# Performance work log

Measured on AMD Instinct MI355X. Metric: run time of the kernel, lower is better.

## Reference

```python
import jax, jax.numpy as jnp
import numpy as np

B, C, H = 256, 5, 13
N_AGENTS = 8192
N_EDGES = 262144
ACT = 21


def setup_inputs() -> dict:
    key = jax.random.key(0)
    ks = jax.random.split(key, 20)
    inp = {
        "x": jax.random.normal(ks[0], (B, C, H, H), jnp.float32),
        "x_msg": jax.random.normal(ks[1], (N_AGENTS,), jnp.float32),
        "edge_index": jax.random.randint(ks[2], (N_EDGES, 2), 0, N_AGENTS, jnp.int64 if jax.config.jax_enable_x64 else jnp.int32),
        "action": jax.random.randint(ks[3], (B,), 0, ACT, jnp.int32),
        # params (orthogonal init approximated by scaled normal; math identical)
        "conv1_w": jax.random.normal(ks[4], (32, 5, 3, 3), jnp.float32) * 0.1,
        "conv1_b": jnp.zeros((32,), jnp.float32),
        "conv2_w": jax.random.normal(ks[5], (64, 32, 3, 3), jnp.float32) * 0.05,
        "conv2_b": jnp.zeros((64,), jnp.float32),
        "fc_w": jax.random.normal(ks[6], (512, 1024), jnp.float32) * 0.03,
        "fc_b": jnp.zeros((512,), jnp.float32),
        "fc_mu_w": jax.random.normal(ks[7], (ACT, 512), jnp.float32) * 0.01,
        "fc_mu_b": jnp.zeros((ACT,), jnp.float32),
        "msg_w": jax.random.normal(ks[8], (N_AGENTS, 512), jnp.float32) * 0.01,
        "msg_b": jnp.zeros((N_AGENTS,), jnp.float32),
        "gcn1_w": jax.random.normal(ks[9], (2, 16), jnp.float32) * 0.5,
        "gcn1_b": jnp.zeros((16,), jnp.float32),
        "gcn2_w": jax.random.normal(ks[10], (16, N_AGENTS), jnp.float32) * 0.1,
        "gcn2_b": jnp.zeros((N_AGENTS,), jnp.float32),
    }
    return inp


def _gcn_norm(edge_index, n):
    # add self-loops; edge_index is (E,2) [src, dst]
    loops = jnp.arange(n, dtype=edge_index.dtype)
    src = jnp.concatenate([edge_index[:, 0], loops])
    dst = jnp.concatenate([edge_index[:, 1], loops])
    deg = jax.ops.segment_sum(jnp.ones_like(src, jnp.float32), dst, num_segments=n)
    dinv = jnp.where(deg > 0, jax.lax.rsqrt(deg), 0.0)
    norm = dinv[src] * dinv[dst]  # [E+n]
    return src, dst, norm


def _gcn_conv(h, src, dst, norm, W, b, n):
    hw = h @ W  # [n, out]
    out = jax.ops.segment_sum(norm[:, None] * hw[src], dst, num_segments=n)
    return out + b


def reference(x, x_msg, edge_index, action, conv1_w, conv1_b, conv2_w, conv2_b,
              fc_w, fc_b, fc_mu_w, fc_mu_b, msg_w, msg_b,
              gcn1_w, gcn1_b, gcn2_w, gcn2_b):
    dn = ("NCHW", "OIHW", "NCHW")
    h = jax.lax.conv_general_dilated(x, conv1_w, (2, 2), "VALID", dimension_numbers=dn)
    h = jax.nn.relu(h + conv1_b[None, :, None, None])  # [B,32,6,6]
    h = jax.lax.conv_general_dilated(h, conv2_w, (1, 1), "VALID", dimension_numbers=dn)
    h = jax.nn.relu(h + conv2_b[None, :, None, None])  # [B,64,4,4]
    h = h.reshape(h.shape[0], -1)  # [B,1024], torch NCHW flatten order
    hidden = jax.nn.relu(h @ fc_w.T + fc_b)  # [B,512]

    logits = hidden @ fc_mu_w.T + fc_mu_b            # [B,21]
    actor_encoding = hidden @ msg_w.T + msg_b        # [B,N]

    # Categorical log_prob / entropy for the given action
    logp = jax.nn.log_softmax(logits, axis=-1)
    log_prob = jnp.take_along_axis(logp, action[:, None], axis=1)[:, 0]
    entropy = -jnp.sum(jnp.exp(logp) * logp, axis=-1)

    # GNN message branch (eval mode: dropout is identity)
    feats = jnp.stack([x_msg, actor_encoding[0]], axis=0).T  # [N,2]
    n = feats.shape[0]
    src, dst, norm = _gcn_norm(edge_index, n)
    g = jax.nn.relu(_gcn_conv(feats, src, dst, norm, gcn1_w, gcn1_b, n))  # [N,16]
    g = _gcn_conv(g, src, dst, norm, gcn2_w, gcn2_b, n)                    # [N,N]
    msg_out = jax.nn.log_softmax(g, axis=1).mean(axis=1)                   # [N]

    return (action, msg_out, log_prob, entropy)
```

## Files before the change

kernel.cpp:

```cpp
#include <hip/hip_runtime.h>
#include <hip/hip_bf16.h>

#define NB 256
#define NACT 21
#define NA 8192
#define NE 262144
#define CSR_CAP 128
#define LOG2E 1.44269504f

#if __has_builtin(__builtin_amdgcn_exp2f)
#define EXP2F(x) __builtin_amdgcn_exp2f(x)
#else
#define EXP2F(x) exp2f(x)
#endif

typedef __attribute__((ext_vector_type(8))) short short8;
typedef __attribute__((ext_vector_type(4))) float float4v;

__device__ inline float wsum64(float v) {
#pragma unroll
  for (int m = 32; m > 0; m >>= 1) v += __shfl_xor(v, m, 64);
  return v;
}

__device__ inline unsigned short f2bf(float f) {
  union { __hip_bfloat16 h; unsigned short u; } cv;
  cv.h = __float2bfloat16(f);
  return cv.u;
}

__global__ void k_init(const int* action, int* cnt, float* out) {
  int i = blockIdx.x * 256 + threadIdx.x;
  if (i < NA) cnt[i] = 0;
  if (i < NB) out[i] = (float)action[i];
}

__global__ __launch_bounds__(512, 4) void k_prep(
    const int* __restrict__ edges, const float* __restrict__ fcw,
    const float* __restrict__ g2w, const float* __restrict__ g2b,
    unsigned short* fcwbf, unsigned short* w2t, float* wpart, int* cnt, int* csr) {
  __shared__ float red[16][17];
  __shared__ float b2s[16];
  int t = threadIdx.x, blk = blockIdx.x;
  {
    int e = blk * 512 + t;
    int s = edges[2 * e], d = edges[2 * e + 1];
    int slot = atomicAdd(&cnt[d], 1);
    if (slot < CSR_CAP) csr[d * CSR_CAP + slot] = s;
  }
  {
    int base = (blk * 512 + t) * 2;
    float2 v = *(const float2*)&fcw[base];
    fcwbf[base + 0] = f2bf(v.x);
    fcwbf[base + 1] = f2bf(v.y);
  }
  {
    if (t < 256) {
      int jj = t >> 4, k = t & 15;
      int j = blk * 16 + jj;
      float w = g2w[k * 8192 + j];
      w2t[j * 16 + k] = f2bf(w);
      red[jj][k] = w;
    }
    if (t < 16) b2s[t] = g2b[blk * 16 + t];
    __syncthreads();
    if (t < 16) {
      float s = 0.0f;
#pragma unroll
      for (int q = 0; q < 16; q++) s += red[q][t];
      wpart[blk * 17 + t] = s;
    } else if (t == 16) {
      float s = 0.0f;
#pragma unroll
      for (int q = 0; q < 16; q++) s += b2s[q];
      wpart[blk * 17 + 16] = s;
    }
  }
}

__global__ __launch_bounds__(512, 2) void k_conv(
    const float* __restrict__ x, const float* __restrict__ c1w, const float* __restrict__ c1b,
    const float* __restrict__ c2w, const float* __restrict__ c2b, unsigned short* h1024bf) {
  __shared__ float xs[845];
  __shared__ float w1s[1440];
  __shared__ float c1s[1152];
  __shared__ float w2s[64 * 73];
  int t = threadIdx.x, blk = blockIdx.x;
  for (int i = t; i < 845; i += 512) xs[i] = x[blk * 845 + i];
  for (int i = t; i < 1440; i += 512) w1s[i] = c1w[i];
  __syncthreads();
  for (int idx = t; idx < 1152; idx += 512) {
    int oc = idx / 36, p = idx - oc * 36;
    int oy = p / 6, ox = p - oy * 6;
    float acc = c1b[oc];
    const float* wp = &w1s[oc * 45];
#pragma unroll
    for (int ic = 0; ic < 5; ic++)
#pragma unroll
      for (int ky = 0; ky < 3; ky++)
#pragma unroll
        for (int kx = 0; kx < 3; kx++)
          acc += xs[ic * 169 + (oy * 2 + ky) * 13 + ox * 2 + kx] * wp[ic * 9 + ky * 3 + kx];
    c1s[idx] = fmaxf(acc, 0.0f);
  }
  int p = t & 15, oc2 = t >> 4;
  int oy = p >> 2, ox = p & 3;
  float a0 = c2b[oc2 * 2 + 0], a1 = c2b[oc2 * 2 + 1];
  for (int icb = 0; icb < 32; icb += 8) {
    __syncthreads();
    for (int i = t; i < 4608; i += 512) {
      int oc = i / 72, r = i - oc * 72;
      w2s[oc * 73 + r] = c2w[oc * 288 + icb * 9 + r];
    }
    __syncthreads();
#pragma unroll
    for (int ic = 0; ic < 8; ic++) {
#pragma unroll
      for (int ky = 0; ky < 3; ky++) {
#pragma unroll
        for (int kx = 0; kx < 3; kx++) {
          float cvv = c1s[(icb + ic) * 36 + (oy + ky) * 6 + ox + kx];
          int wi = ic * 9 + ky * 3 + kx;
          a0 += cvv * w2s[(oc2 * 2 + 0) * 73 + wi];
          a1 += cvv * w2s[(oc2 * 2 + 1) * 73 + wi];
        }
      }
    }
  }
  unsigned short* hp = &h1024bf[blk * 1024];
  hp[(oc2 * 2 + 0) * 16 + p] = f2bf(fmaxf(a0, 0.0f));
  hp[(oc2 * 2 + 1) * 16 + p] = f2bf(fmaxf(a1, 0.0f));
}

__global__ __launch_bounds__(256, 4) void k_fc(
    const int* __restrict__ cnt, const float* __restrict__ x_msg,
    const unsigned short* __restrict__ h1024bf, const unsigned short* __restrict__ fcwbf,
    const float* __restrict__ fcb, float* hidden, float* dinv, float* xs2) {
  __shared__ float red[4][256];
  int t = threadIdx.x, blk = blockIdx.x;
  int wave = t >> 6, lane = t & 63;
  if (blk < 32) {
    int i = blk * 256 + t;
    float d = rsqrtf((float)cnt[i] + 1.0f);
    dinv[i] = d;
    xs2[i] = d * x_msg[i];
  }
  int tr = blk >> 5, tc = blk & 31;
  int m = lane & 15, quad = lane >> 4;
  const unsigned short* ap = &h1024bf[(tr * 16 + m) * 1024 + wave * 256 + quad * 8];
  const unsigned short* bp = &fcwbf[(tc * 16 + m) * 1024 + wave * 256 + quad * 8];
  float4v acc = {0.0f, 0.0f, 0.0f, 0.0f};
#pragma unroll
  for (int i = 0; i < 8; i++) {
    short8 a = *(const short8*)(ap + i * 32);
    short8 b = *(const short8*)(bp + i * 32);
    acc = __builtin_amdgcn_mfma_f32_16x16x32_bf16(a, b, acc, 0, 0, 0);
  }
#pragma unroll
  for (int r = 0; r < 4; r++) red[wave][(quad * 4 + r) * 16 + m] = acc[r];
  __syncthreads();
  {
    float s = red[0][t] + red[1][t] + red[2][t] + red[3][t];
    int gr = tr * 16 + (t >> 4);
    int gc = tc * 16 + (t & 15);
    hidden[gr * 512 + gc] = fmaxf(s + fcb[gc], 0.0f);
  }
}

__global__ __launch_bounds__(512, 2) void k_he(
    const float* __restrict__ hidden, const float* __restrict__ muw,
    const float* __restrict__ mub, const float* __restrict__ msgw,
    const float* __restrict__ msgb, const float* __restrict__ dinv,
    float* es2, float* out) {
  __shared__ float muT[10752];
  __shared__ float hrows[2048];
  int t = threadIdx.x, blk = blockIdx.x;
  int wave = t >> 6, lane = t & 63;
  if (blk < 64) {
    int b0 = blk * 4;
    for (int i = t; i < 10752; i += 512) {
      int a = i >> 9, k = i & 511;
      muT[k * 21 + a] = muw[i];
    }
    for (int i = t; i < 2048; i += 512) hrows[i] = hidden[b0 * 512 + i];
    __syncthreads();
    if (wave < 4) {
      int b = b0 + wave;
      float logit = -1e30f;
      if (lane < NACT) {
        float acc = mub[lane];
        const float* hr = &hrows[wave * 512];
        for (int k = 0; k < 512; k++) acc += hr[k] * muT[k * 21 + lane];
        logit = acc;
      }
      float m = logit;
#pragma unroll
      for (int s = 32; s > 0; s >>= 1) m = fmaxf(m, __shfl_xor(m, s, 64));
      float e = (lane < NACT) ? __expf(logit - m) : 0.0f;
      float se = wsum64(e);
      float swl = wsum64(e * logit);
      float lse = m + __logf(se);
      if (lane == 0) out[8704 + b] = lse - swl / se;
      int act = (int)out[b];
      if (lane == act) out[8448 + b] = logit - lse;
    }
  } else {
    int wg = (blk - 64) * 8 + wave;
    for (int j = wg; j < NA; j += 3584) {
      const float* wp = &msgw[j * 512 + lane * 8];
      float4 w0 = *(const float4*)(wp);
      float4 w1 = *(const float4*)(wp + 4);
      float4 h0 = *(const float4*)&hidden[lane * 8];
      float4 h1 = *(const float4*)&hidden[lane * 8 + 4];
      float s = w0.x * h0.x + w0.y * h0.y + w0.z * h0.z + w0.w * h0.w +
                w1.x * h1.x + w1.y * h1.y + w1.z * h1.z + w1.w * h1.w;
      s = wsum64(s);
      if (lane == 0) es2[j] = dinv[j] * (s + msgb[j]);
    }
  }
}

__global__ __launch_bounds__(512, 4) void k_g1(
    const int* __restrict__ cnt, const int* __restrict__ csr,
    const float* __restrict__ dinv, const float* __restrict__ xs2,
    const float* __restrict__ es2, const float* __restrict__ g1w,
    const float* __restrict__ g1b, float* gbuf2) {
  int t = threadIdx.x, blk = blockIdx.x;
  int wave = t >> 6, lane = t & 63;
  int wg = blk * 8 + wave;
#pragma unroll
  for (int rr = 0; rr < 2; rr++) {
    int i = wg * 2 + rr;
    int ci = min(cnt[i], CSR_CAP);
    float di = dinv[i];
    float a0 = 0.0f, a1 = 0.0f;
    for (int e = lane; e < ci; e += 64) {
      int s = csr[i * CSR_CAP + e];
      a0 += xs2[s];
      a1 += es2[s];
    }
    float f0 = (wsum64(a0) + xs2[i]) * di;
    float f1 = (wsum64(a1) + es2[i]) * di;
    if (lane < 16) {
      float gv = fmaxf(f0 * g1w[lane] + f1 * g1w[16 + lane] + g1b[lane], 0.0f);
      gbuf2[i * 16 + lane] = di * gv;
    }
  }
}

__global__ __launch_bounds__(512, 2) void k_msg(
    const int* __restrict__ cnt, const int* __restrict__ csr,
    const float* __restrict__ dinv, const float* __restrict__ gbuf2,
    const float* __restrict__ wpart, const unsigned short* __restrict__ w2t,
    const float* __restrict__ g2b, float* out) {
  __shared__ __align__(16) unsigned short vbf[512];
  __shared__ float vf[512];
  __shared__ float pl[4096];
  __shared__ float sl[256];
  __shared__ float wp[16][17];
  __shared__ float wsf[17];
  int t = threadIdx.x, blk = blockIdx.x;
  int wave = t >> 6, lane = t & 63;
  int rowbase = blk * 32;
  {
    int eq = lane >> 4, c = lane & 15;
#pragma unroll
    for (int rr = 0; rr < 4; rr++) {
      int il = wave * 4 + rr;
      int i = rowbase + il;
      int ci = min(cnt[i], CSR_CAP);
      float di = dinv[i];
      float acc = (eq == 0) ? gbuf2[i * 16 + c] : 0.0f;
      for (int e = eq; e < ci; e += 4) {
        int s = csr[i * CSR_CAP + e];
        acc += gbuf2[s * 16 + c];
      }
      acc *= di;
      acc += __shfl_xor(acc, 16, 64);
      acc += __shfl_xor(acc, 32, 64);
      if (eq == 0) {
        vf[il * 16 + c] = acc;
        vbf[il * 16 + c] = f2bf(acc * LOG2E);
      }
    }
  }
  __syncthreads();
  if (t < 272) {
    int bq = t / 17, k = t - bq * 17;
    float s = 0.0f;
    for (int b = bq; b < 512; b += 16) s += wpart[b * 17 + k];
    wp[bq][k] = s;
  }
  __syncthreads();
  if (t < 17) {
    float s = 0.0f;
#pragma unroll
    for (int q = 0; q < 16; q++) s += wp[q][t];
    wsf[t] = s;
  }
  __syncthreads();
  float myMean = 0.0f;
  if (t < 32) {
    float dot = 0.0f;
#pragma unroll
    for (int c = 0; c < 16; c++) dot += vf[t * 16 + c] * wsf[c];
    myMean = (dot + wsf[16]) * (1.0f / 8192.0f);
  }
  {
    int quad = lane >> 4, n = lane & 15;
    int k8 = quad * 8;
    short8 za = {0, 0, 0, 0, 0, 0, 0, 0};
    short8 a1 = za, a2 = za;
    if (quad < 2) {
      a1 = *(const short8*)&vbf[n * 16 + k8];
      a2 = *(const short8*)&vbf[(16 + n) * 16 + k8];
    }
    float sacc[8];
#pragma unroll
    for (int q = 0; q < 8; q++) sacc[q] = 0.0f;
    int colb = wave * 1024 + n;
    for (int tp = 0; tp < 64; tp += 2) {
      int col1 = colb + tp * 16;
      int col2 = col1 + 16;
      short8 b1 = za, b2 = za;
      if (quad < 2) {
        b1 = *(const short8*)&w2t[col1 * 16 + k8];
        b2 = *(const short8*)&w2t[col2 * 16 + k8];
      }
      float bb1 = g2b[col1] * LOG2E, bb2 = g2b[col2] * LOG2E;
      float4v c1 = {bb1, bb1, bb1, bb1};
      float4v c2 = {bb2, bb2, bb2, bb2};
      float4v s11 = __builtin_amdgcn_mfma_f32_16x16x32_bf16(a1, b1, c1, 0, 0, 0);
      float4v s21 = __builtin_amdgcn_mfma_f32_16x16x32_bf16(a2, b1, c1, 0, 0, 0);
      float4v s12 = __builtin_amdgcn_mfma_f32_16x16x32_bf16(a1, b2, c2, 0, 0, 0);
      float4v s22 = __builtin_amdgcn_mfma_f32_16x16x32_bf16(a2, b2, c2, 0, 0, 0);
#pragma unroll
      for (int r = 0; r < 4; r++) {
        sacc[r]     += EXP2F(s11[r]) + EXP2F(s12[r]);
        sacc[4 + r] += EXP2F(s21[r]) + EXP2F(s22[r]);
      }
    }
#pragma unroll
    for (int q = 0; q < 8; q++) {
      int rl = (q >> 2) * 16 + quad * 4 + (q & 3);
      pl[rl * 128 + wave * 16 + n] = sacc[q];
    }
  }
  __syncthreads();
  if (t < 256) {
    int r = t >> 3, seg = t & 7;
    int base = r * 128 + seg * 16;
    float ll = 0.0f;
#pragma unroll
    for (int i = 0; i < 16; i++) ll += pl[base + i];
    sl[r * 8 + seg] = ll;
  }
  __syncthreads();
  if (t < 32) {
    float ll = 0.0f;
#pragma unroll
    for (int i = 0; i < 8; i++) ll += sl[t * 8 + i];
    out[256 + rowbase + t] = myMean - __logf(ll);
  }
}

extern "C" void kernel_launch(void* const* d_in, const int* in_sizes, int n_in,
                              void* d_out, int out_size, void* d_ws, size_t ws_size,
                              hipStream_t stream) {
  const float* x     = (const float*)d_in[0];
  const float* x_msg = (const float*)d_in[1];
  const int*   edges = (const int*)d_in[2];
  const int*   action= (const int*)d_in[3];
  const float* c1w   = (const float*)d_in[4];
  const float* c1b   = (const float*)d_in[5];
  const float* c2w   = (const float*)d_in[6];
  const float* c2b   = (const float*)d_in[7];
  const float* fcw   = (const float*)d_in[8];
  const float* fcb   = (const float*)d_in[9];
  const float* muw   = (const float*)d_in[10];
  const float* mub   = (const float*)d_in[11];
  const float* msgw  = (const float*)d_in[12];
  const float* msgb  = (const float*)d_in[13];
  const float* g1w   = (const float*)d_in[14];
  const float* g1b   = (const float*)d_in[15];
  const float* g2w   = (const float*)d_in[16];
  const float* g2b   = (const float*)d_in[17];
  float* out = (float*)d_out;

  float* ws     = (float*)d_ws;
  unsigned short* h1024bf = (unsigned short*)ws;
  unsigned short* fcwbf   = (unsigned short*)(ws + 131072);
  float* hidden = ws + 393216;
  float* es2    = ws + 524288;
  float* dinv   = ws + 532480;
  float* xs2    = ws + 540672;
  float* gbuf2  = ws + 548864;
  float* wpart  = ws + 679936;
  unsigned short* w2t = (unsigned short*)(ws + 688640);
  int*   cnt    = (int*)(ws + 754176);
  int*   csr    = (int*)(ws + 762368);

  k_init<<<33, 256, 0, stream>>>(action, cnt, out);
  k_prep<<<512, 512, 0, stream>>>(edges, fcw, g2w, g2b, fcwbf, w2t, wpart, cnt, csr);
  k_conv<<<256, 512, 0, stream>>>(x, c1w, c1b, c2w, c2b, h1024bf);
  k_fc  <<<512, 256, 0, stream>>>(cnt, x_msg, h1024bf, fcwbf, fcb, hidden, dinv, xs2);
  k_he  <<<512, 512, 0, stream>>>(hidden, muw, mub, msgw, msgb, dinv, es2, out);
  k_g1  <<<512, 512, 0, stream>>>(cnt, csr, dinv, xs2, es2, g1w, g1b, gbuf2);
  k_msg <<<256, 512, 0, stream>>>(cnt, csr, dinv, gbuf2, wpart, w2t, g2b, out);
}
```

Before: 188.0 us.

## Merge prep and conv kernels, split CSR into two half-lists, halve conv blocks

Fuses the edge-bucketing/weight-conversion prep kernel with the conv kernel into one launch, where blocks 0-511 each compute half of an image's conv2 outputs and blocks 512-767 do the prep work. Each prep thread now handles two edges. These go into separate per-node counters and two 64-slot halves of the CSR row, which spreads atomic contention across two counters per node. Gather loops in g1 and msg read both halves. This removes one kernel launch and raises conv parallelism, at the cost of a larger union shared-memory footprint and capping each half list at 64 neighbours.

After: 330.1 us. 1.76x slower.

```diff
diff --git a/kernel.cpp b/kernel.cpp
--- a/kernel.cpp
+++ b/kernel.cpp
@@ -5,7 +5,7 @@
 #define NACT 21
 #define NA 8192
 #define NE 262144
-#define CSR_CAP 128
+#define HCAP 64
 #define LOG2E 1.44269504f
 
 #if __has_builtin(__builtin_amdgcn_exp2f)
@@ -29,111 +29,110 @@
   return cv.u;
 }
 
-__global__ void k_init(const int* action, int* cnt, float* out) {
+__global__ void k_init(const int* action, int* cnt2, float* out) {
   int i = blockIdx.x * 256 + threadIdx.x;
-  if (i < NA) cnt[i] = 0;
+  if (i < 2 * NA) cnt2[i] = 0;
   if (i < NB) out[i] = (float)action[i];
 }
 
-__global__ __launch_bounds__(512, 4) void k_prep(
-    const int* __restrict__ edges, const float* __restrict__ fcw,
-    const float* __restrict__ g2w, const float* __restrict__ g2b,
-    unsigned short* fcwbf, unsigned short* w2t, float* wpart, int* cnt, int* csr) {
-  __shared__ float red[16][17];
-  __shared__ float b2s[16];
+__global__ __launch_bounds__(512, 4) void k_pc(
+    const float* __restrict__ x, const int* __restrict__ edges,
+    const float* __restrict__ c1w, const float* __restrict__ c1b,
+    const float* __restrict__ c2w, const float* __restrict__ c2b,
+    const float* __restrict__ fcw, const float* __restrict__ g2w,
+    const float* __restrict__ g2b,
+    unsigned short* h1024bf, unsigned short* fcwbf, unsigned short* w2t,
+    float* wpart, int* cnt2, int* csr) {
+  union SM {
+    struct { float xs[845]; float w1s[1440]; float c1s[1152]; float w2s[32 * 73]; } cv;
+    struct { float red[32][17]; float b2s[32]; } w2;
+  };
+  __shared__ __align__(16) union SM sm;
   int t = threadIdx.x, blk = blockIdx.x;
-  {
-    int e = blk * 512 + t;
-    int s = edges[2 * e], d = edges[2 * e + 1];
-    int slot = atomicAdd(&cnt[d], 1);
-    if (slot < CSR_CAP) csr[d * CSR_CAP + slot] = s;
-  }
-  {
-    int base = (blk * 512 + t) * 2;
-    float2 v = *(const float2*)&fcw[base];
-    fcwbf[base + 0] = f2bf(v.x);
-    fcwbf[base + 1] = f2bf(v.y);
-  }
-  {
-    if (t < 256) {
+
+  if (blk >= 512) {
+    int pb = blk - 512;
+    {
+      int e = pb * 512 + t;
+      int s = edges[2 * e], d = edges[2 * e + 1];
+      int slot = atomicAdd(&cnt2[2 * d], 1);
+      if (slot < HCAP) csr[d * 128 + slot] = s;
+      int e2 = e + 131072;
+      s = edges[2 * e2]; d = edges[2 * e2 + 1];
+      slot = atomicAdd(&cnt2[2 * d + 1], 1);
+      if (slot < HCAP) csr[d * 128 + HCAP + slot] = s;
+    }
+    {
+      int base = (pb * 512 + t) * 4;
+      float4 v = *(const float4*)&fcw[base];
+      fcwbf[base + 0] = f2bf(v.x); fcwbf[base + 1] = f2bf(v.y);
+      fcwbf[base + 2] = f2bf(v.z); fcwbf[base + 3] = f2bf(v.w);
+    }
+    {
       int jj = t >> 4, k = t & 15;
-      int j = blk * 16 + jj;
+      int j = pb * 32 + jj;
       float w = g2w[k * 8192 + j];
       w2t[j * 16 + k] = f2bf(w);
-      red[jj][k] = w;
-    }
-    if (t < 16) b2s[t] = g2b[blk * 16 + t];
-    __syncthreads();
-    if (t < 16) {
-      float s = 0.0f;
-#pragma unroll
-      for (int q = 0; q < 16; q++) s += red[q][t];
-      wpart[blk * 17 + t] = s;
-    } else if (t == 16) {
-      float s = 0.0f;
-#pragma unroll
-      for (int q = 0; q < 16; q++) s += b2s[q];
-      wpart[blk * 17 + 16] = s;
-    }
-  }
-}
-
-__global__ __launch_bounds__(512, 2) void k_conv(
-    const float* __restrict__ x, const float* __restrict__ c1w, const float* __restrict__ c1b,
-    const float* __restrict__ c2w, const float* __restrict__ c2b, unsigned short* h1024bf) {
-  __shared__ float xs[845];
-  __shared__ float w1s[1440];
-  __shared__ float c1s[1152];
-  __shared__ float w2s[64 * 73];
-  int t = threadIdx.x, blk = blockIdx.x;
-  for (int i = t; i < 845; i += 512) xs[i] = x[blk * 845 + i];
-  for (int i = t; i < 1440; i += 512) w1s[i] = c1w[i];
+      sm.w2.red[jj][k] = w;
+      if (t < 32) sm.w2.b2s[t] = g2b[pb * 32 + t];
+      __syncthreads();
+      if (t < 16) {
+        float s = 0.0f;
+#pragma unroll
+        for (int q = 0; q < 32; q++) s += sm.w2.red[q][t];
+        wpart[pb * 17 + t] = s;
+      } else if (t == 16) {
+        float s = 0.0f;
+#pragma unroll
+        for (int q = 0; q < 32; q++) s += sm.w2.b2s[q];
+        wpart[pb * 17 + 16] = s;
+      }
+    }
+    return;
+  }
+  int img = blk >> 1, half = blk & 1;
+  for (int i = t; i < 845; i += 512) sm.cv.xs[i] = x[img * 845 + i];
+  for (int i = t; i < 1440; i += 512) sm.cv.w1s[i] = c1w[i];
   __syncthreads();
   for (int idx = t; idx < 1152; idx += 512) {
     int oc = idx / 36, p = idx - oc * 36;
     int oy = p / 6, ox = p - oy * 6;
     float acc = c1b[oc];
-    const float* wp = &w1s[oc * 45];
+    const float* wp = &sm.cv.w1s[oc * 45];
 #pragma unroll
     for (int ic = 0; ic < 5; ic++)
 #pragma unroll
       for (int ky = 0; ky < 3; ky++)
 #pragma unroll
         for (int kx = 0; kx < 3; kx++)
-          acc += xs[ic * 169 + (oy * 2 + ky) * 13 + ox * 2 + kx] * wp[ic * 9 + ky * 3 + kx];
-    c1s[idx] = fmaxf(acc, 0.0f);
-  }
-  int p = t & 15, oc2 = t >> 4;
+          acc += sm.cv.xs[ic * 169 + (oy * 2 + ky) * 13 + ox * 2 + kx] * wp[ic * 9 + ky * 3 + kx];
+    sm.cv.c1s[idx] = fmaxf(acc, 0.0f);
+  }
+  int p = t & 15, ocl = t >> 4;
+  int oc = half * 32 + ocl;
   int oy = p >> 2, ox = p & 3;
-  float a0 = c2b[oc2 * 2 + 0], a1 = c2b[oc2 * 2 + 1];
+  float a0 = c2b[oc];
   for (int icb = 0; icb < 32; icb += 8) {
     __syncthreads();
-    for (int i = t; i < 4608; i += 512) {
-      int oc = i / 72, r = i - oc * 72;
-      w2s[oc * 73 + r] = c2w[oc * 288 + icb * 9 + r];
+    for (int i = t; i < 2304; i += 512) {
+      int o = i / 72, r = i - o * 72;
+      sm.cv.w2s[o * 73 + r] = c2w[(half * 32 + o) * 288 + icb * 9 + r];
     }
     __syncthreads();
 #pragma unroll
-    for (int ic = 0; ic < 8; ic++) {
-#pragma unroll
-      for (int ky = 0; ky < 3; ky++) {
-#pragma unroll
-        for (int kx = 0; kx < 3; kx++) {
-          float cvv = c1s[(icb + ic) * 36 + (oy + ky) * 6 + ox + kx];
-          int wi = ic * 9 + ky * 3 + kx;
-          a0 += cvv * w2s[(oc2 * 2 + 0) * 73 + wi];
-          a1 += cvv * w2s[(oc2 * 2 + 1) * 73 + wi];
-        }
-      }
-    }
-  }
-  unsigned short* hp = &h1024bf[blk * 1024];
-  hp[(oc2 * 2 + 0) * 16 + p] = f2bf(fmaxf(a0, 0.0f));
-  hp[(oc2 * 2 + 1) * 16 + p] = f2bf(fmaxf(a1, 0.0f));
+    for (int ic = 0; ic < 8; ic++)
+#pragma unroll
+      for (int ky = 0; ky < 3; ky++)
+#pragma unroll
+        for (int kx = 0; kx < 3; kx++)
+          a0 += sm.cv.c1s[(icb + ic) * 36 + (oy + ky) * 6 + ox + kx] *
+                sm.cv.w2s[ocl * 73 + ic * 9 + ky * 3 + kx];
+  }
+  h1024bf[img * 1024 + oc * 16 + p] = f2bf(fmaxf(a0, 0.0f));
 }
 
 __global__ __launch_bounds__(256, 4) void k_fc(
-    const int* __restrict__ cnt, const float* __restrict__ x_msg,
+    const int* __restrict__ cnt2, const float* __restrict__ x_msg,
     const unsigned short* __restrict__ h1024bf, const unsigned short* __restrict__ fcwbf,
     const float* __restrict__ fcb, float* hidden, float* dinv, float* xs2) {
   __shared__ float red[4][256];
@@ -141,7 +140,7 @@
   int wave = t >> 6, lane = t & 63;
   if (blk < 32) {
     int i = blk * 256 + t;
-    float d = rsqrtf((float)cnt[i] + 1.0f);
+    float d = rsqrtf((float)(cnt2[2 * i] + cnt2[2 * i + 1]) + 1.0f);
     dinv[i] = d;
     xs2[i] = d * x_msg[i];
   }
@@ -221,7 +220,7 @@
 }
 
 __global__ __launch_bounds__(512, 4) void k_g1(
-    const int* __restrict__ cnt, const int* __restrict__ csr,
+    const int* __restrict__ cnt2, const int* __restrict__ csr,
     const float* __restrict__ dinv, const float* __restrict__ xs2,
     const float* __restrict__ es2, const float* __restrict__ g1w,
     const float* __restrict__ g1b, float* gbuf2) {
@@ -231,11 +230,16 @@
 #pragma unroll
   for (int rr = 0; rr < 2; rr++) {
     int i = wg * 2 + rr;
-    int ci = min(cnt[i], CSR_CAP);
+    int ci0 = min(cnt2[2 * i], HCAP), ci1 = min(cnt2[2 * i + 1], HCAP);
     float di = dinv[i];
     float a0 = 0.0f, a1 = 0.0f;
-    for (int e = lane; e < ci; e += 64) {
-      int s = csr[i * CSR_CAP + e];
+    if (lane < ci0) {
+      int s = csr[i * 128 + lane];
+      a0 += xs2[s];
+      a1 += es2[s];
+    }
+    if (lane < ci1) {
+      int s = csr[i * 128 + HCAP + lane];
       a0 += xs2[s];
       a1 += es2[s];
     }
@@ -249,7 +253,7 @@
 }
 
 __global__ __launch_bounds__(512, 2) void k_msg(
-    const int* __restrict__ cnt, const int* __restrict__ csr,
+    const int* __restrict__ cnt2, const int* __restrict__ csr,
     const float* __restrict__ dinv, const float* __restrict__ gbuf2,
     const float* __restrict__ wpart, const unsigned short* __restrict__ w2t,
     const float* __restrict__ g2b, float* out) {
@@ -268,11 +272,15 @@
     for (int rr = 0; rr < 4; rr++) {
       int il = wave * 4 + rr;
       int i = rowbase + il;
-      int ci = min(cnt[i], CSR_CAP);
+      int ci0 = min(cnt2[2 * i], HCAP), ci1 = min(cnt2[2 * i + 1], HCAP);
       float di = dinv[i];
       float acc = (eq == 0) ? gbuf2[i * 16 + c] : 0.0f;
-      for (int e = eq; e < ci; e += 4) {
-        int s = csr[i * CSR_CAP + e];
+      for (int e = eq; e < ci0; e += 4) {
+        int s = csr[i * 128 + e];
+        acc += gbuf2[s * 16 + c];
+      }
+      for (int e = eq; e < ci1; e += 4) {
+        int s = csr[i * 128 + HCAP + e];
         acc += gbuf2[s * 16 + c];
       }
       acc *= di;
@@ -288,7 +296,7 @@
   if (t < 272) {
     int bq = t / 17, k = t - bq * 17;
     float s = 0.0f;
-    for (int b = bq; b < 512; b += 16) s += wpart[b * 17 + k];
+    for (int b = bq; b < 256; b += 16) s += wpart[b * 17 + k];
     wp[bq][k] = s;
   }
   __syncthreads();
@@ -396,15 +404,15 @@
   float* xs2    = ws + 540672;
   float* gbuf2  = ws + 548864;
   float* wpart  = ws + 679936;
-  unsigned short* w2t = (unsigned short*)(ws + 688640);
-  int*   cnt    = (int*)(ws + 754176);
-  int*   csr    = (int*)(ws + 762368);
-
-  k_init<<<33, 256, 0, stream>>>(action, cnt, out);
-  k_prep<<<512, 512, 0, stream>>>(edges, fcw, g2w, g2b, fcwbf, w2t, wpart, cnt, csr);
-  k_conv<<<256, 512, 0, stream>>>(x, c1w, c1b, c2w, c2b, h1024bf);
-  k_fc  <<<512, 256, 0, stream>>>(cnt, x_msg, h1024bf, fcwbf, fcb, hidden, dinv, xs2);
+  unsigned short* w2t = (unsigned short*)(ws + 684288);
+  int*   cnt2   = (int*)(ws + 749824);
+  int*   csr    = (int*)(ws + 766208);
+
+  k_init<<<64, 256, 0, stream>>>(action, cnt2, out);
+  k_pc  <<<768, 512, 0, stream>>>(x, edges, c1w, c1b, c2w, c2b, fcw, g2w, g2b,
+                                  h1024bf, fcwbf, w2t, wpart, cnt2, csr);
+  k_fc  <<<512, 256, 0, stream>>>(cnt2, x_msg, h1024bf, fcwbf, fcb, hidden, dinv, xs2);
   k_he  <<<512, 512, 0, stream>>>(hidden, muw, mub, msgw, msgb, dinv, es2, out);
-  k_g1  <<<512, 512, 0, stream>>>(cnt, csr, dinv, xs2, es2, g1w, g1b, gbuf2);
-  k_msg <<<256, 512, 0, stream>>>(cnt, csr, dinv, gbuf2, wpart, w2t, g2b, out);
-}
+  k_g1  <<<512, 512, 0, stream>>>(cnt2, csr, dinv, xs2, es2, g1w, g1b, gbuf2);
+  k_msg <<<256, 512, 0, stream>>>(cnt2, csr, dinv, gbuf2, wpart, w2t, g2b, out);
+}
```

## Split edge counters into two halves and split conv2 across two blocks per image

Applied to the files above, without the earlier changes.

Edge insertion now uses two per-node counters, one per half of the edge list, each with its own 64-slot CSR segment. This reduces atomic contention and lets k_g1 gather each row without a loop. Separately, k_conv launches two blocks per image, each computing 32 output channels, which doubles the block count and halves the weight staging per block. The cost is that conv1 is computed twice per image, and a node can now hit the per-half cap of 64 entries, which makes overflow handling stricter than the old shared cap of 128.

New measurement: 257.3 us. 1.37x slower.

```diff
diff --git a/kernel.cpp b/kernel.cpp
--- a/kernel.cpp
+++ b/kernel.cpp
@@ -5,7 +5,7 @@
 #define NACT 21
 #define NA 8192
 #define NE 262144
-#define CSR_CAP 128
+#define HCAP 64
 #define LOG2E 1.44269504f
 
 #if __has_builtin(__builtin_amdgcn_exp2f)
@@ -29,24 +29,25 @@
   return cv.u;
 }
 
-__global__ void k_init(const int* action, int* cnt, float* out) {
+__global__ void k_init(const int* action, int* cnt2, float* out) {
   int i = blockIdx.x * 256 + threadIdx.x;
-  if (i < NA) cnt[i] = 0;
+  if (i < 2 * NA) cnt2[i] = 0;
   if (i < NB) out[i] = (float)action[i];
 }
 
 __global__ __launch_bounds__(512, 4) void k_prep(
     const int* __restrict__ edges, const float* __restrict__ fcw,
     const float* __restrict__ g2w, const float* __restrict__ g2b,
-    unsigned short* fcwbf, unsigned short* w2t, float* wpart, int* cnt, int* csr) {
+    unsigned short* fcwbf, unsigned short* w2t, float* wpart, int* cnt2, int* csr) {
   __shared__ float red[16][17];
   __shared__ float b2s[16];
   int t = threadIdx.x, blk = blockIdx.x;
   {
     int e = blk * 512 + t;
+    int half = e >> 17;
     int s = edges[2 * e], d = edges[2 * e + 1];
-    int slot = atomicAdd(&cnt[d], 1);
-    if (slot < CSR_CAP) csr[d * CSR_CAP + slot] = s;
+    int slot = atomicAdd(&cnt2[2 * d + half], 1);
+    if (slot < HCAP) csr[d * 128 + half * HCAP + slot] = s;
   }
   {
     int base = (blk * 512 + t) * 2;
@@ -84,9 +85,10 @@
   __shared__ float xs[845];
   __shared__ float w1s[1440];
   __shared__ float c1s[1152];
-  __shared__ float w2s[64 * 73];
-  int t = threadIdx.x, blk = blockIdx.x;
-  for (int i = t; i < 845; i += 512) xs[i] = x[blk * 845 + i];
+  __shared__ float w2s[32 * 73];
+  int t = threadIdx.x, blk = blockIdx.x;
+  int img = blk >> 1, half = blk & 1;
+  for (int i = t; i < 845; i += 512) xs[i] = x[img * 845 + i];
   for (int i = t; i < 1440; i += 512) w1s[i] = c1w[i];
   __syncthreads();
   for (int idx = t; idx < 1152; idx += 512) {
@@ -103,37 +105,31 @@
           acc += xs[ic * 169 + (oy * 2 + ky) * 13 + ox * 2 + kx] * wp[ic * 9 + ky * 3 + kx];
     c1s[idx] = fmaxf(acc, 0.0f);
   }
-  int p = t & 15, oc2 = t >> 4;
+  int p = t & 15, ocl = t >> 4;
+  int oc = half * 32 + ocl;
   int oy = p >> 2, ox = p & 3;
-  float a0 = c2b[oc2 * 2 + 0], a1 = c2b[oc2 * 2 + 1];
+  float a0 = c2b[oc];
   for (int icb = 0; icb < 32; icb += 8) {
     __syncthreads();
-    for (int i = t; i < 4608; i += 512) {
-      int oc = i / 72, r = i - oc * 72;
-      w2s[oc * 73 + r] = c2w[oc * 288 + icb * 9 + r];
+    for (int i = t; i < 2304; i += 512) {
+      int o = i / 72, r = i - o * 72;
+      w2s[o * 73 + r] = c2w[(half * 32 + o) * 288 + icb * 9 + r];
     }
     __syncthreads();
 #pragma unroll
-    for (int ic = 0; ic < 8; ic++) {
-#pragma unroll
-      for (int ky = 0; ky < 3; ky++) {
-#pragma unroll
-        for (int kx = 0; kx < 3; kx++) {
-          float cvv = c1s[(icb + ic) * 36 + (oy + ky) * 6 + ox + kx];
-          int wi = ic * 9 + ky * 3 + kx;
-          a0 += cvv * w2s[(oc2 * 2 + 0) * 73 + wi];
-          a1 += cvv * w2s[(oc2 * 2 + 1) * 73 + wi];
-        }
-      }
-    }
-  }
-  unsigned short* hp = &h1024bf[blk * 1024];
-  hp[(oc2 * 2 + 0) * 16 + p] = f2bf(fmaxf(a0, 0.0f));
-  hp[(oc2 * 2 + 1) * 16 + p] = f2bf(fmaxf(a1, 0.0f));
+    for (int ic = 0; ic < 8; ic++)
+#pragma unroll
+      for (int ky = 0; ky < 3; ky++)
+#pragma unroll
+        for (int kx = 0; kx < 3; kx++)
+          a0 += c1s[(icb + ic) * 36 + (oy + ky) * 6 + ox + kx] *
+                w2s[ocl * 73 + ic * 9 + ky * 3 + kx];
+  }
+  h1024bf[img * 1024 + oc * 16 + p] = f2bf(fmaxf(a0, 0.0f));
 }
 
 __global__ __launch_bounds__(256, 4) void k_fc(
-    const int* __restrict__ cnt, const float* __restrict__ x_msg,
+    const int* __restrict__ cnt2, const float* __restrict__ x_msg,
     const unsigned short* __restrict__ h1024bf, const unsigned short* __restrict__ fcwbf,
     const float* __restrict__ fcb, float* hidden, float* dinv, float* xs2) {
   __shared__ float red[4][256];
@@ -141,7 +137,7 @@
   int wave = t >> 6, lane = t & 63;
   if (blk < 32) {
     int i = blk * 256 + t;
-    float d = rsqrtf((float)cnt[i] + 1.0f);
+    float d = rsqrtf((float)(cnt2[2 * i] + cnt2[2 * i + 1]) + 1.0f);
     dinv[i] = d;
     xs2[i] = d * x_msg[i];
   }
@@ -221,7 +217,7 @@
 }
 
 __global__ __launch_bounds__(512, 4) void k_g1(
-    const int* __restrict__ cnt, const int* __restrict__ csr,
+    const int* __restrict__ cnt2, const int* __restrict__ csr,
     const float* __restrict__ dinv, const float* __restrict__ xs2,
     const float* __restrict__ es2, const float* __restrict__ g1w,
     const float* __restrict__ g1b, float* gbuf2) {
@@ -231,11 +227,16 @@
 #pragma unroll
   for (int rr = 0; rr < 2; rr++) {
     int i = wg * 2 + rr;
-    int ci = min(cnt[i], CSR_CAP);
+    int ci0 = min(cnt2[2 * i], HCAP), ci1 = min(cnt2[2 * i + 1], HCAP);
     float di = dinv[i];
     float a0 = 0.0f, a1 = 0.0f;
-    for (int e = lane; e < ci; e += 64) {
-      int s = csr[i * CSR_CAP + e];
+    if (lane < ci0) {
+      int s = csr[i * 128 + lane];
+      a0 += xs2[s];
+      a1 += es2[s];
+    }
+    if (lane < ci1) {
+      int s = csr[i * 128 + HCAP + lane];
       a0 += xs2[s];
       a1 += es2[s];
     }
@@ -249,7 +250,7 @@
 }
 
 __global__ __launch_bounds__(512, 2) void k_msg(
-    const int* __restrict__ cnt, const int* __restrict__ csr,
+    const int* __restrict__ cnt2, const int* __restrict__ csr,
     const float* __restrict__ dinv, const float* __restrict__ gbuf2,
     const float* __restrict__ wpart, const unsigned short* __restrict__ w2t,
     const float* __restrict__ g2b, float* out) {
@@ -268,11 +269,15 @@
     for (int rr = 0; rr < 4; rr++) {
       int il = wave * 4 + rr;
       int i = rowbase + il;
-      int ci = min(cnt[i], CSR_CAP);
+      int ci0 = min(cnt2[2 * i], HCAP), ci1 = min(cnt2[2 * i + 1], HCAP);
       float di = dinv[i];
       float acc = (eq == 0) ? gbuf2[i * 16 + c] : 0.0f;
-      for (int e = eq; e < ci; e += 4) {
-        int s = csr[i * CSR_CAP + e];
+      for (int e = eq; e < ci0; e += 4) {
+        int s = csr[i * 128 + e];
+        acc += gbuf2[s * 16 + c];
+      }
+      for (int e = eq; e < ci1; e += 4) {
+        int s = csr[i * 128 + HCAP + e];
         acc += gbuf2[s * 16 + c];
       }
       acc *= di;
@@ -397,14 +402,14 @@
   float* gbuf2  = ws + 548864;
   float* wpart  = ws + 679936;
   unsigned short* w2t = (unsigned short*)(ws + 688640);
-  int*   cnt    = (int*)(ws + 754176);
-  int*   csr    = (int*)(ws + 762368);
-
-  k_init<<<33, 256, 0, stream>>>(action, cnt, out);
-  k_prep<<<512, 512, 0, stream>>>(edges, fcw, g2w, g2b, fcwbf, w2t, wpart, cnt, csr);
-  k_conv<<<256, 512, 0, stream>>>(x, c1w, c1b, c2w, c2b, h1024bf);
-  k_fc  <<<512, 256, 0, stream>>>(cnt, x_msg, h1024bf, fcwbf, fcb, hidden, dinv, xs2);
+  int*   cnt2   = (int*)(ws + 754176);
+  int*   csr    = (int*)(ws + 770560);
+
+  k_init<<<64, 256, 0, stream>>>(action, cnt2, out);
+  k_prep<<<512, 512, 0, stream>>>(edges, fcw, g2w, g2b, fcwbf, w2t, wpart, cnt2, csr);
+  k_conv<<<512, 512, 0, stream>>>(x, c1w, c1b, c2w, c2b, h1024bf);
+  k_fc  <<<512, 256, 0, stream>>>(cnt2, x_msg, h1024bf, fcwbf, fcb, hidden, dinv, xs2);
   k_he  <<<512, 512, 0, stream>>>(hidden, muw, mub, msgw, msgb, dinv, es2, out);
-  k_g1  <<<512, 512, 0, stream>>>(cnt, csr, dinv, xs2, es2, g1w, g1b, gbuf2);
-  k_msg <<<256, 512, 0, stream>>>(cnt, csr, dinv, gbuf2, wpart, w2t, g2b, out);
-}
+  k_g1  <<<512, 512, 0, stream>>>(cnt2, csr, dinv, xs2, es2, g1w, g1b, gbuf2);
+  k_msg <<<256, 512, 0, stream>>>(cnt2, csr, dinv, gbuf2, wpart, w2t, g2b, out);
+}
```
